# Kernel optimization log

Hardware: AMD Instinct MI355X
Metric: run time of the kernel (lower is better)

The kernel has to match this reference:

```python
import jax, jax.numpy as jnp
import numpy as np
from jax import lax

B, N, C = 4, 20000, 256
NUM_VIEW = 300
NUM_SAMPLE = 1024
EPS_BN = 1e-5


def _grasp_views(n=NUM_VIEW):
    # graspnetAPI generate_grasp_views: spiral points on unit sphere
    phi = (np.sqrt(5.0) - 1.0) / 2.0
    i = np.arange(n)
    z = (2.0 * i + 1.0) / n - 1.0
    r = np.sqrt(np.maximum(1.0 - z * z, 0.0))
    x = r * np.cos(2.0 * np.pi * i * phi)
    y = r * np.sin(2.0 * np.pi * i * phi)
    return jnp.asarray(np.stack([x, y, z], axis=1).astype(np.float32))  # [300,3]

_TEMPLATE_VIEWS = _grasp_views()


def _conv1x1(x, w, b):
    # Conv1d with kernel_size=1: x [B,Cin,N], w [Cout,Cin], b [Cout]
    return jnp.einsum('oc,bcn->bon', w, x) + b[None, :, None]


def _bn_eval(x, g, be, m, v):
    # BatchNorm1d in eval mode (running stats)
    scale = g / jnp.sqrt(v + EPS_BN)
    return x * scale[None, :, None] + (be - m * scale)[None, :, None]


def _masked_fps(xyz, mask, n_samples):
    # Equivalent to compacting valid points, running torch furthest_point_sample,
    # and mapping indices back: run FPS on the full set with invalid points pinned
    # to -inf min-distance so they are never selected. Start = first valid index
    # (index 0 of the compacted set). Tie-breaking matches (order preserved).
    first = jnp.argmax(mask, axis=1)                      # [B]
    init_d = jnp.where(mask, jnp.float32(1e10), -jnp.inf)  # [B,N]

    def step(carry, _):
        dists, last = carry
        p = jnp.take_along_axis(xyz, last[:, None, None], axis=1)  # [B,1,3]
        d = jnp.sum((xyz - p) ** 2, axis=-1)                       # [B,N]
        dists = jnp.minimum(dists, d)
        nxt = jnp.argmax(dists, axis=1)
        return (dists, nxt), nxt

    _, rest = lax.scan(step, (init_d, first), None, length=n_samples - 1)
    return jnp.concatenate([first[None, :], rest], axis=0).T  # [B,S] int


def _viewpoint_to_matrix(towards):
    # batch_viewpoint_params_to_matrix with batch_angle = 0 => R1 = I
    ax = towards  # [M,3]
    ay = jnp.stack([-ax[:, 1], ax[:, 0], jnp.zeros_like(ax[:, 0])], axis=-1)
    deg = jnp.sum(ay * ay, axis=-1, keepdims=True) == 0
    ay = jnp.where(deg, jnp.array([0.0, 1.0, 0.0], dtype=ax.dtype), ay)
    nx = ax / jnp.linalg.norm(ax, axis=-1, keepdims=True)
    ny = ay / jnp.linalg.norm(ay, axis=-1, keepdims=True)
    nz = jnp.cross(nx, ny)
    return jnp.stack([nx, ny, nz], axis=-1)  # [M,3,3], axes as columns


def setup_inputs() -> dict:
    key = jax.random.key(0)
    ks = jax.random.split(key, 18)

    def w(k, shape, s=0.05):
        return jax.random.normal(k, shape, jnp.float32) * s

    return dict(
        seed_xyz=jax.random.normal(ks[0], (B, N, 3), jnp.float32),
        seed_features=jax.random.normal(ks[1], (B, C, N), jnp.float32),
        gh_w1=w(ks[2], (C, C)), gh_b1=w(ks[3], (C,), 0.01),
        gh_g=1.0 + 0.1 * jax.random.normal(ks[4], (C,), jnp.float32),
        gh_be=w(ks[5], (C,), 0.01),
        gh_m=w(ks[6], (C,), 0.1),
        gh_v=jax.random.uniform(ks[7], (C,), jnp.float32, 0.5, 1.5),
        gh_w2=w(ks[8], (3, C)), gh_b2=w(ks[9], (3,), 0.01),
        c1_w=w(ks[10], (C, C)), c1_b=w(ks[11], (C,), 0.01),
        bn_g=1.0 + 0.1 * jax.random.normal(ks[12], (C,), jnp.float32),
        bn_b=w(ks[13], (C,), 0.01),
        bn_m=w(ks[14], (C,), 0.1),
        bn_v=jax.random.uniform(ks[15], (C,), jnp.float32, 0.5, 1.5),
        c2_w=w(ks[16], (3, C)), c2_b=w(ks[17], (3,), 0.01),
    )


def reference(seed_xyz, seed_features, gh_w1, gh_b1, gh_g, gh_be, gh_m, gh_v,
              gh_w2, gh_b2, c1_w, c1_b, bn_g, bn_b, bn_m, bn_v, c2_w, c2_b):
    # graspable head: conv-BN-ReLU-conv -> [B,3,N]
    h = jax.nn.relu(_bn_eval(_conv1x1(seed_features, gh_w1, gh_b1), gh_g, gh_be, gh_m, gh_v))
    graspable = _conv1x1(h, gh_w2, gh_b2)
    objectness_score = graspable[:, :2]          # [B,2,N]
    graspness_score = graspable[:, 2]            # [B,N]

    obj_mask = jnp.argmax(objectness_score, axis=1) == 1
    gmask = (graspness_score > 0.1) & obj_mask   # [B,N] bool

    graspable_inds = _masked_fps(seed_xyz, gmask, NUM_SAMPLE)            # [B,S]
    graspable_xyz = jnp.take_along_axis(seed_xyz, graspable_inds[:, :, None], axis=1)   # [B,S,3]
    graspable_features = jnp.take_along_axis(seed_features, graspable_inds[:, None, :], axis=2)  # [B,C,S]
    fp2_graspness = jnp.take_along_axis(graspness_score, graspable_inds, axis=1)        # [B,S]

    f = jax.nn.relu(_bn_eval(_conv1x1(graspable_features, c1_w, c1_b), bn_g, bn_b, bn_m, bn_v))
    vp_xyz = jnp.transpose(_conv1x1(f, c2_w, c2_b), (0, 2, 1))  # [B,S,3]

    # cosine similarity against 300 template views (torch clamps each norm at 1e-8)
    vn = vp_xyz / jnp.maximum(jnp.linalg.norm(vp_xyz, axis=-1, keepdims=True), 1e-8)
    tn = _TEMPLATE_VIEWS / jnp.maximum(jnp.linalg.norm(_TEMPLATE_VIEWS, axis=-1, keepdims=True), 1e-8)
    cos = jnp.einsum('bsd,vd->bsv', vn, tn)      # [B,S,300]
    top_view_inds = jnp.argmax(cos, axis=2)      # [B,S]

    vp_rot = _viewpoint_to_matrix(-vp_xyz.reshape(-1, 3)).reshape(B, NUM_SAMPLE, 3, 3)

    return (objectness_score, graspness_score, graspable_xyz, graspable_inds,
            graspable_features, fp2_graspness, vp_xyz, top_view_inds, vp_rot)
```

## Files before the change

kernel.cpp:

```cpp
#include <hip/hip_runtime.h>
#include <hip/hip_bf16.h>
#include <math.h>

static constexpr int BB = 4;
static constexpr int NN = 20000;
static constexpr int CC = 256;
static constexpr int SS = 1024;
static constexpr int NV = 300;

static constexpr size_t O0 = 0;
static constexpr size_t O1 = O0 + (size_t)BB*2*NN;
static constexpr size_t O2 = O1 + (size_t)BB*NN;
static constexpr size_t O3 = O2 + (size_t)BB*SS*3;
static constexpr size_t O4 = O3 + (size_t)BB*SS;
static constexpr size_t O5 = O4 + (size_t)BB*CC*SS;
static constexpr size_t O6 = O5 + (size_t)BB*SS;
static constexpr size_t O7 = O6 + (size_t)BB*SS*3;
static constexpr size_t O8 = O7 + (size_t)BB*SS;

typedef float v2f __attribute__((ext_vector_type(2)));

static constexpr int TN = 64;
static constexpr int KC = 32;
static constexpr int SW_LD = 260;
static constexpr int PS_LD = 68;

__global__ __launch_bounds__(256, 2) void gemm_fused(
    const float* __restrict__ X,
    const float* __restrict__ W1, const float* __restrict__ B1v,
    const float* __restrict__ Gv, const float* __restrict__ BEv,
    const float* __restrict__ Mv, const float* __restrict__ Vv,
    const float* __restrict__ W2, const float* __restrict__ B2v,
    float* __restrict__ o0, float* __restrict__ o1)
{
    __shared__ alignas(16) char smem_raw[KC*SW_LD*4 + KC*TN*4];
    float* sW   = (float*)smem_raw;
    float* sF   = (float*)(smem_raw + KC*SW_LD*4);
    float* psum = (float*)smem_raw;
    float* gout = (float*)(smem_raw + 3*32*PS_LD*4);

    const int t  = threadIdx.x;
    const int b  = blockIdx.y;
    const int n0 = blockIdx.x * TN;
    const int tm = t & 31;
    const int tn = t >> 5;

    const float* Xb = X + (size_t)b * CC * NN;

    float acc[8][8];
#pragma unroll
    for (int i = 0; i < 8; ++i)
#pragma unroll
        for (int j = 0; j < 8; ++j) acc[i][j] = 0.f;

    for (int k0 = 0; k0 < CC; k0 += KC) {
#pragma unroll
        for (int r = 0; r < (CC*KC)/256; ++r) {
            int idx = r*256 + t;
            int m  = idx >> 5;
            int kk = idx & 31;
            sW[kk*SW_LD + m] = W1[m*CC + k0 + kk];
        }
#pragma unroll
        for (int r = 0; r < (KC*TN)/256; ++r) {
            int idx = r*256 + t;
            int kk = idx >> 6;
            int j  = idx & 63;
            int col = n0 + j;
            float v = 0.f;
            if (col < NN) v = Xb[(size_t)(k0+kk)*NN + col];
            sF[kk*TN + j] = v;
        }
        __syncthreads();
#pragma unroll 8
        for (int kk = 0; kk < KC; ++kk) {
            const float4 a0 = *(const float4*)(sW + kk*SW_LD + tm*8);
            const float4 a1 = *(const float4*)(sW + kk*SW_LD + tm*8 + 4);
            const float4 f0 = *(const float4*)(sF + kk*TN + tn*8);
            const float4 f1 = *(const float4*)(sF + kk*TN + tn*8 + 4);
            float av[8] = {a0.x,a0.y,a0.z,a0.w,a1.x,a1.y,a1.z,a1.w};
            float bv[8] = {f0.x,f0.y,f0.z,f0.w,f1.x,f1.y,f1.z,f1.w};
#pragma unroll
            for (int i = 0; i < 8; ++i)
#pragma unroll
                for (int j = 0; j < 8; ++j)
                    acc[i][j] = fmaf(av[i], bv[j], acc[i][j]);
        }
        __syncthreads();
    }

    float part[3][8];
#pragma unroll
    for (int r = 0; r < 3; ++r)
#pragma unroll
        for (int j = 0; j < 8; ++j) part[r][j] = 0.f;

#pragma unroll
    for (int i = 0; i < 8; ++i) {
        int m = tm*8 + i;
        float scale = __fdiv_rn(Gv[m], __fsqrt_rn(__fadd_rn(Vv[m], 1e-5f)));
        float shift = __fsub_rn(BEv[m], __fmul_rn(Mv[m], scale));
        float w0 = W2[m], w1 = W2[CC + m], w2 = W2[2*CC + m];
        float b1m = B1v[m];
#pragma unroll
        for (int j = 0; j < 8; ++j) {
            float x = __fadd_rn(acc[i][j], b1m);
            float y = __fadd_rn(__fmul_rn(x, scale), shift);
            float h = y > 0.f ? y : 0.f;
            part[0][j] = fmaf(w0, h, part[0][j]);
            part[1][j] = fmaf(w1, h, part[1][j]);
            part[2][j] = fmaf(w2, h, part[2][j]);
        }
    }
#pragma unroll
    for (int r = 0; r < 3; ++r) {
        float4 p0 = {part[r][0], part[r][1], part[r][2], part[r][3]};
        float4 p1 = {part[r][4], part[r][5], part[r][6], part[r][7]};
        *(float4*)(psum + (r*32 + tm)*PS_LD + tn*8)     = p0;
        *(float4*)(psum + (r*32 + tm)*PS_LD + tn*8 + 4) = p1;
    }
    __syncthreads();
    if (t < 192) {
        int r = t >> 6, col = t & 63;
        float s = 0.f;
#pragma unroll
        for (int w = 0; w < 32; ++w) s = __fadd_rn(s, psum[(r*32 + w)*PS_LD + col]);
        float tot = __fadd_rn(s, B2v[r]);
        gout[r*64 + col] = tot;
    }
    __syncthreads();
    if (t < 64) {
        int n = n0 + t;
        if (n < NN) {
            o0[(size_t)b*2*NN + n]      = gout[t];
            o0[(size_t)b*2*NN + NN + n] = gout[64 + t];
            o1[(size_t)b*NN + n]        = gout[128 + t];
        }
    }
}

static constexpr int FPS_T = 256;
static constexpr int KAMAX = 20;
static constexpr int CAPA  = FPS_T * KAMAX;

template<int CTRL>
__device__ __forceinline__ unsigned long long dpp_umax(unsigned long long k) {
    int lo = __builtin_amdgcn_update_dpp(0, (int)(unsigned)k,         CTRL, 0xf, 0xf, false);
    int hi = __builtin_amdgcn_update_dpp(0, (int)(unsigned)(k >> 32), CTRL, 0xf, 0xf, false);
    unsigned long long ok = ((unsigned long long)(unsigned)hi << 32) | (unsigned)lo;
    return ok > k ? ok : k;
}

__device__ __forceinline__ unsigned long long wave_umax_dpp(unsigned long long k) {
    k = dpp_umax<0x111>(k);
    k = dpp_umax<0x112>(k);
    k = dpp_umax<0x114>(k);
    k = dpp_umax<0x118>(k);
    k = dpp_umax<0x142>(k);
    k = dpp_umax<0x143>(k);
    return k;
}

__device__ __forceinline__ unsigned long long pack_key(float v, int i) {
    unsigned long long k = (((unsigned long long)__float_as_uint(v)) << 32)
                         | (unsigned long long)(0xFFFFFFFFu - (unsigned)i);
    return (v == -INFINITY) ? 0ull : k;
}

template<int KP>
__device__ __forceinline__ void fps_scan_loop(
    int cnt, const float* __restrict__ sxyz,
    unsigned long long (*swk)[4], int* __restrict__ whist)
{
#pragma clang fp contract(off)
    const int t = threadIdx.x;
    const int wave = t >> 6, lane = t & 63;

    v2f X2[KP], Y2[KP], Z2[KP], D2[KP];
#pragma unroll
    for (int jp = 0; jp < KP; ++jp) {
        int g0 = t + ((2*jp) << 8);
        int g1 = g0 + 256;
        bool v0 = g0 < cnt, v1 = g1 < cnt;
        float4 wa = v0 ? *(const float4*)&sxyz[g0*4] : make_float4(0.f,0.f,0.f,0.f);
        float4 wb = v1 ? *(const float4*)&sxyz[g1*4] : make_float4(0.f,0.f,0.f,0.f);
        X2[jp][0] = wa.x; X2[jp][1] = wb.x;
        Y2[jp][0] = wa.y; Y2[jp][1] = wb.y;
        Z2[jp][0] = wa.z; Z2[jp][1] = wb.z;
        D2[jp][0] = v0 ? 1e10f : -INFINITY;
        D2[jp][1] = v1 ? 1e10f : -INFINITY;
    }

    float px = sxyz[0], py = sxyz[1], pz = sxyz[2];

    for (int it = 1; it < SS; ++it) {
        float bv = -INFINITY; int bi = 0x7fffffff;
#pragma unroll
        for (int jp = 0; jp < KP; ++jp) {
            v2f dx = X2[jp] - px;
            v2f dy = Y2[jp] - py;
            v2f dz = Z2[jp] - pz;
            v2f xx = dx*dx, yy = dy*dy;
            v2f sxy = xx + yy;
            v2f zz = dz*dz;
            v2f dd = sxy + zz;
            float dn0 = fminf(D2[jp][0], dd[0]);
            float dn1 = fminf(D2[jp][1], dd[1]);
            D2[jp][0] = dn0;
            D2[jp][1] = dn1;
            if (dn0 > bv) { bv = dn0; bi = t + ((2*jp)   << 8); }
            if (dn1 > bv) { bv = dn1; bi = t + ((2*jp+1) << 8); }
        }
        unsigned long long key = wave_umax_dpp(pack_key(bv, bi));
        int par = it & 1;
        if (lane == 63) swk[par][wave] = key;
        __syncthreads();
        const ulonglong2* kp = (const ulonglong2*)&swk[par][0];
        ulonglong2 kA = kp[0], kB = kp[1];
        unsigned long long m0 = kA.x > kA.y ? kA.x : kA.y;
        unsigned long long m1 = kB.x > kB.y ? kB.x : kB.y;
        unsigned long long best = m0 > m1 ? m0 : m1;
        int wi = (int)(0xFFFFFFFFu - (unsigned)(best & 0xFFFFFFFFull));
        float4 w4 = *(const float4*)&sxyz[wi*4];
        px = w4.x; py = w4.y; pz = w4.z;
        if (t == 0) whist[it] = wi;
    }
}

__global__ __launch_bounds__(256, 1) void mega_kernel(
    const float* __restrict__ xyz, const float* __restrict__ feats,
    const float* __restrict__ o0, const float* __restrict__ o1,
    const float* __restrict__ c1w, const float* __restrict__ c1b,
    const float* __restrict__ bng, const float* __restrict__ bnb,
    const float* __restrict__ bnm, const float* __restrict__ bnv,
    const float* __restrict__ c2w, const float* __restrict__ c2b,
    int* __restrict__ corig, float* __restrict__ cxg,
    float* __restrict__ cyg, float* __restrict__ czg,
    float* __restrict__ o2, float* __restrict__ o3, float* __restrict__ o4,
    float* __restrict__ o5, float* __restrict__ o6, float* __restrict__ o7,
    float* __restrict__ o8, int* __restrict__ indsp, int* __restrict__ donep)
{
    __shared__ alignas(16) char sm[86272];
    const int t = threadIdx.x;
    const int wave = t >> 6, lane = t & 63;

    if (blockIdx.x < BB) {
        const int b = blockIdx.x;
        const size_t bofs = (size_t)b*NN;
        float* sxyz = (float*)sm;
        int*   whist = (int*)(sm + 81920);
        unsigned long long (*swk)[4] = (unsigned long long (*)[4])(sm + 86016);
        int*   wsum  = (int*)(sm + 86080);
        int*   smisc = (int*)(sm + 86096);

        if (t == 0) smisc[0] = 0;
        __syncthreads();
        const float* ob0 = o0 + (size_t)b*2*NN;
        const float* ob1 = o1 + (size_t)b*NN;
        for (int base = 0; base < NN; base += 256) {
            int i = base + t;
            bool valid = i < NN;
            float g1 = valid ? ob1[i]      : 0.f;
            float v0 = valid ? ob0[i]      : 0.f;
            float v1 = valid ? ob0[NN + i] : 0.f;
            bool m = valid && (g1 > 0.1f) && (v1 > v0);
            unsigned long long bal = __ballot(m);
            int pre = __popcll(bal & ((1ull << lane) - 1ull));
            if (lane == 0) wsum[wave] = __popcll(bal);
            __syncthreads();
            int offs = smisc[0];
            int tilesum = wsum[0] + wsum[1] + wsum[2] + wsum[3];
            for (int ww = 0; ww < wave; ++ww) offs += wsum[ww];
            if (m) {
                int pos = offs + pre;
                float x = xyz[(bofs + i)*3 + 0];
                float y = xyz[(bofs + i)*3 + 1];
                float z = xyz[(bofs + i)*3 + 2];
                corig[bofs + pos] = i;
                cxg[bofs + pos] = x; cyg[bofs + pos] = y; czg[bofs + pos] = z;
                if (pos < CAPA) {
                    float4 w4 = {x, y, z, 0.f};
                    *(float4*)&sxyz[pos*4] = w4;
                }
            }
            __syncthreads();
            if (t == 0) smisc[0] += tilesum;
        }
        __syncthreads();
        const int cnt = smisc[0];

        float* o3b = o3 + (size_t)b*SS;
        int*   oib = indsp + (size_t)b*SS;

        if (cnt <= 0) {
            for (int s = t; s < SS; s += FPS_T) { o3b[s] = 0.f; oib[s] = 0; }
            __syncthreads();
            if (t == 0) {
                __threadfence();
                __hip_atomic_fetch_add(donep, 1, __ATOMIC_RELEASE, __HIP_MEMORY_SCOPE_AGENT);
            }
            return;
        }

        if (t == 0) whist[0] = 0;
        __syncthreads();

        if (cnt <= CAPA) {
            int kat2 = ((cnt + 255) >> 8);
            kat2 = (kat2 + 1) & ~1;
            int kpn = kat2 >> 1;
            switch (kpn) {
                case 1:  fps_scan_loop<1 >(cnt, sxyz, swk, whist); break;
                case 2:  fps_scan_loop<2 >(cnt, sxyz, swk, whist); break;
                case 3:  fps_scan_loop<3 >(cnt, sxyz, swk, whist); break;
                case 4:  fps_scan_loop<4 >(cnt, sxyz, swk, whist); break;
                case 5:  fps_scan_loop<5 >(cnt, sxyz, swk, whist); break;
                case 6:  fps_scan_loop<6 >(cnt, sxyz, swk, whist); break;
                case 7:  fps_scan_loop<7 >(cnt, sxyz, swk, whist); break;
                case 8:  fps_scan_loop<8 >(cnt, sxyz, swk, whist); break;
                case 9:  fps_scan_loop<9 >(cnt, sxyz, swk, whist); break;
                default: fps_scan_loop<10>(cnt, sxyz, swk, whist); break;
            }
        } else {
            float* Dl = sxyz;
            for (int g = t; g < cnt; g += FPS_T) Dl[g] = 1e10f;
            __syncthreads();
            float px = cxg[bofs], py = cyg[bofs], pz = czg[bofs];
            for (int it = 1; it < SS; ++it) {
                float bv = -INFINITY; int bi = 0x7fffffff;
                for (int g = t; g < cnt; g += FPS_T) {
                    float dx = __fsub_rn(cxg[bofs + g], px);
                    float dy = __fsub_rn(cyg[bofs + g], py);
                    float dz = __fsub_rn(czg[bofs + g], pz);
                    float d  = __fadd_rn(__fadd_rn(__fmul_rn(dx,dx), __fmul_rn(dy,dy)), __fmul_rn(dz,dz));
                    float dn = fminf(Dl[g], d);
                    Dl[g] = dn;
                    if (dn > bv) { bv = dn; bi = g; }
                }
                unsigned long long key = wave_umax_dpp(pack_key(bv, bi));
                int par = it & 1;
                if (lane == 63) swk[par][wave] = key;
                __syncthreads();
                const ulonglong2* kp = (const ulonglong2*)&swk[par][0];
                ulonglong2 kA = kp[0], kB = kp[1];
                unsigned long long m0 = kA.x > kA.y ? kA.x : kA.y;
                unsigned long long m1 = kB.x > kB.y ? kB.x : kB.y;
                unsigned long long best = m0 > m1 ? m0 : m1;
                int wi = (int)(0xFFFFFFFFu - (unsigned)(best & 0xFFFFFFFFull));
                px = cxg[bofs + wi]; py = cyg[bofs + wi]; pz = czg[bofs + wi];
                if (t == 0) whist[it] = wi;
            }
        }

        __syncthreads();
        for (int s = t; s < SS; s += FPS_T) {
            int wi  = whist[s];
            int org = corig[bofs + wi];
            oib[s] = org;
            o3b[s] = (float)org;
        }
        __syncthreads();
        if (t == 0) {
            __threadfence();
            __hip_atomic_fetch_add(donep, 1, __ATOMIC_RELEASE, __HIP_MEMORY_SCOPE_AGENT);
        }
        return;
    }

    {
        int* smisc = (int*)(sm + 86096);
        if (t == 0) smisc[1] = 0;
        __syncthreads();
        float a = 1.0f + (float)t * 1e-6f, bmul = 1.0000001f, c = 0.f;
        for (int iter = 0; iter < (1 << 22); ++iter) {
#pragma unroll
            for (int u = 0; u < 16; ++u) c = fmaf(a, bmul, c);
            __builtin_amdgcn_s_sleep(8);
            if (t == 0 && (iter & 7) == 0) {
                if (__hip_atomic_load(donep, __ATOMIC_RELAXED, __HIP_MEMORY_SCOPE_AGENT) >= BB)
                    *(volatile int*)&smisc[1] = 1;
            }
            if (*(volatile int*)&smisc[1]) break;
        }
        ((volatile float*)sm)[32 + (t & 31)] = c;
        __syncthreads();
        (void)__hip_atomic_load(donep, __ATOMIC_ACQUIRE, __HIP_MEMORY_SCOPE_AGENT);
    }

    const int wid = blockIdx.x - BB;

    if (wid < 64) {
        const int bi = wid >> 4;
        const int n0 = (wid & 15) << 6;
        float* sW   = (float*)sm;
        float* sF   = (float*)(sm + KC*SW_LD*4);
        float* psum = (float*)sm;
        float* gout = (float*)(sm + 3*32*PS_LD*4);
        float* tv   = (float*)(sm + KC*SW_LD*4);
        int*   sIdx = (int*)(sm + 81920);

        if (t < 64) sIdx[t] = indsp[(bi << 10) + n0 + t];
        __syncthreads();

        const int tm = t & 31;
        const int tn = t >> 5;

        float acc[8][8];
#pragma unroll
        for (int i = 0; i < 8; ++i)
#pragma unroll
            for (int j = 0; j < 8; ++j) acc[i][j] = 0.f;

        for (int k0 = 0; k0 < CC; k0 += KC) {
#pragma unroll
            for (int r = 0; r < (CC*KC)/256; ++r) {
                int idx = r*256 + t;
                int m  = idx >> 5;
                int kk = idx & 31;
                sW[kk*SW_LD + m] = c1w[m*CC + k0 + kk];
            }
#pragma unroll
            for (int r = 0; r < (KC*TN)/256; ++r) {
                int idx = r*256 + t;
                int kk = idx >> 6;
                int j  = idx & 63;
                sF[kk*TN + j] = feats[((size_t)bi*CC + k0 + kk)*NN + sIdx[j]];
            }
            __syncthreads();
#pragma unroll 8
            for (int kk = 0; kk < KC; ++kk) {
                const float4 a0 = *(const float4*)(sW + kk*SW_LD + tm*8);
                const float4 a1 = *(const float4*)(sW + kk*SW_LD + tm*8 + 4);
                const float4 f0 = *(const float4*)(sF + kk*TN + tn*8);
                const float4 f1 = *(const float4*)(sF + kk*TN + tn*8 + 4);
                float av[8] = {a0.x,a0.y,a0.z,a0.w,a1.x,a1.y,a1.z,a1.w};
                float bv[8] = {f0.x,f0.y,f0.z,f0.w,f1.x,f1.y,f1.z,f1.w};
#pragma unroll
                for (int i = 0; i < 8; ++i)
#pragma unroll
                    for (int j = 0; j < 8; ++j)
                        acc[i][j] = fmaf(av[i], bv[j], acc[i][j]);
            }
            __syncthreads();
        }

        float part[3][8];
#pragma unroll
        for (int r = 0; r < 3; ++r)
#pragma unroll
            for (int j = 0; j < 8; ++j) part[r][j] = 0.f;

#pragma unroll
        for (int i = 0; i < 8; ++i) {
            int m = tm*8 + i;
            float scale = __fdiv_rn(bng[m], __fsqrt_rn(__fadd_rn(bnv[m], 1e-5f)));
            float shift = __fsub_rn(bnb[m], __fmul_rn(bnm[m], scale));
            float w0 = c2w[m], w1 = c2w[CC + m], w2 = c2w[2*CC + m];
            float b1m = c1b[m];
#pragma unroll
            for (int j = 0; j < 8; ++j) {
                float x = __fadd_rn(acc[i][j], b1m);
                float y = __fadd_rn(__fmul_rn(x, scale), shift);
                float h = y > 0.f ? y : 0.f;
                part[0][j] = fmaf(w0, h, part[0][j]);
                part[1][j] = fmaf(w1, h, part[1][j]);
                part[2][j] = fmaf(w2, h, part[2][j]);
            }
        }
#pragma unroll
        for (int r = 0; r < 3; ++r) {
            float4 p0 = {part[r][0], part[r][1], part[r][2], part[r][3]};
            float4 p1 = {part[r][4], part[r][5], part[r][6], part[r][7]};
            *(float4*)(psum + (r*32 + tm)*PS_LD + tn*8)     = p0;
            *(float4*)(psum + (r*32 + tm)*PS_LD + tn*8 + 4) = p1;
        }
        __syncthreads();
        if (t < 192) {
            int r = t >> 6, col = t & 63;
            float s = 0.f;
#pragma unroll
            for (int w = 0; w < 32; ++w) s = __fadd_rn(s, psum[(r*32 + w)*PS_LD + col]);
            float tot = __fadd_rn(s, c2b[r]);
            gout[r*64 + col] = tot;
            o6[((size_t)bi*SS + n0 + col)*3 + r] = tot;
        }
        __syncthreads();
        for (int i = t; i < NV; i += 256) {
            double phi = (sqrt(5.0) - 1.0) * 0.5;
            double zd  = (2.0*(double)i + 1.0)/300.0 - 1.0;
            double rr  = sqrt(fmax(1.0 - zd*zd, 0.0));
            double ang = 2.0 * 3.14159265358979323846 * (double)i * phi;
            float fx = (float)(rr * cos(ang));
            float fy = (float)(rr * sin(ang));
            float fz = (float)zd;
            float nr = __fsqrt_rn(__fadd_rn(__fadd_rn(__fmul_rn(fx,fx), __fmul_rn(fy,fy)), __fmul_rn(fz,fz)));
            float dn = fmaxf(nr, 1e-8f);
            tv[i]       = __fdiv_rn(fx, dn);
            tv[NV + i]  = __fdiv_rn(fy, dn);
            tv[2*NV + i]= __fdiv_rn(fz, dn);
        }
        __syncthreads();
        if (t < 64) {
            int col = t;
            int sg = bi*SS + n0 + col;
            float vx = gout[col], vy = gout[64 + col], vz = gout[128 + col];

            float nr = __fsqrt_rn(__fadd_rn(__fadd_rn(__fmul_rn(vx,vx), __fmul_rn(vy,vy)), __fmul_rn(vz,vz)));
            float dn = fmaxf(nr, 1e-8f);
            float ux = __fdiv_rn(vx, dn), uy = __fdiv_rn(vy, dn), uz = __fdiv_rn(vz, dn);
            float best = -INFINITY; int bidx = 0;
            for (int v = 0; v < NV; ++v) {
                float cde = __fadd_rn(__fadd_rn(__fmul_rn(ux, tv[v]), __fmul_rn(uy, tv[NV+v])), __fmul_rn(uz, tv[2*NV+v]));
                if (cde > best) { best = cde; bidx = v; }
            }
            o7[sg] = (float)bidx;

            float axx = -vx, axy = -vy, axz = -vz;
            float ayx = vy, ayy = -vx, ayz = 0.f;
            float s2 = __fadd_rn(__fadd_rn(__fmul_rn(ayx,ayx), __fmul_rn(ayy,ayy)), 0.f);
            if (s2 == 0.f) { ayx = 0.f; ayy = 1.f; ayz = 0.f; }
            float an = __fsqrt_rn(__fadd_rn(__fadd_rn(__fmul_rn(axx,axx), __fmul_rn(axy,axy)), __fmul_rn(axz,axz)));
            float nx0 = __fdiv_rn(axx, an), nx1 = __fdiv_rn(axy, an), nx2 = __fdiv_rn(axz, an);
            float bn2 = __fsqrt_rn(__fadd_rn(__fadd_rn(__fmul_rn(ayx,ayx), __fmul_rn(ayy,ayy)), __fmul_rn(ayz,ayz)));
            float ny0 = __fdiv_rn(ayx, bn2), ny1 = __fdiv_rn(ayy, bn2), ny2 = __fdiv_rn(ayz, bn2);
            float nz0 = __fsub_rn(__fmul_rn(nx1, ny2), __fmul_rn(nx2, ny1));
            float nz1 = __fsub_rn(__fmul_rn(nx2, ny0), __fmul_rn(nx0, ny2));
            float nz2 = __fsub_rn(__fmul_rn(nx0, ny1), __fmul_rn(nx1, ny0));
            size_t o = (size_t)sg * 9;
            o8[o+0] = nx0; o8[o+1] = ny0; o8[o+2] = nz0;
            o8[o+3] = nx1; o8[o+4] = ny1; o8[o+5] = nz1;
            o8[o+6] = nx2; o8[o+7] = ny2; o8[o+8] = nz2;
        }
    } else {
        const int NQ = (BB*CC*SS) / 4;
        for (int q = (wid - 64)*256 + t; q < NQ; q += 188*256) {
            int e = q << 2;
            int b = e >> 18;
            int r = e & ((1 << 18) - 1);
            int c = r >> 10;
            int s = r & 1023;
            int4 i4 = *(const int4*)&indsp[(b << 10) + s];
            const float* fb = feats + ((size_t)b*CC + c)*NN;
            float4 v = { fb[i4.x], fb[i4.y], fb[i4.z], fb[i4.w] };
            *(float4*)&o4[e] = v;
            if (c == 0) {
                const float* gb = o1 + (size_t)b*NN;
                float4 g4 = { gb[i4.x], gb[i4.y], gb[i4.z], gb[i4.w] };
                *(float4*)&o5[(b << 10) + s] = g4;
                const float* xb = xyz + (size_t)b*NN*3;
                float o2buf[12];
                int ii[4] = { i4.x, i4.y, i4.z, i4.w };
#pragma unroll
                for (int k = 0; k < 4; ++k) {
                    o2buf[k*3+0] = xb[(size_t)ii[k]*3 + 0];
                    o2buf[k*3+1] = xb[(size_t)ii[k]*3 + 1];
                    o2buf[k*3+2] = xb[(size_t)ii[k]*3 + 2];
                }
                float* dst = o2 + ((size_t)(b << 10) + s)*3;
                *(float4*)&dst[0] = *(float4*)&o2buf[0];
                *(float4*)&dst[4] = *(float4*)&o2buf[4];
                *(float4*)&dst[8] = *(float4*)&o2buf[8];
            }
        }
    }
}

extern "C" void kernel_launch(void* const* d_in, const int* in_sizes, int n_in,
                              void* d_out, int out_size, void* d_ws, size_t ws_size,
                              hipStream_t stream) {
    const float* xyz   = (const float*)d_in[0];
    const float* feats = (const float*)d_in[1];
    const float* gh_w1 = (const float*)d_in[2];
    const float* gh_b1 = (const float*)d_in[3];
    const float* gh_g  = (const float*)d_in[4];
    const float* gh_be = (const float*)d_in[5];
    const float* gh_m  = (const float*)d_in[6];
    const float* gh_v  = (const float*)d_in[7];
    const float* gh_w2 = (const float*)d_in[8];
    const float* gh_b2 = (const float*)d_in[9];
    const float* c1_w  = (const float*)d_in[10];
    const float* c1_b  = (const float*)d_in[11];
    const float* bn_g  = (const float*)d_in[12];
    const float* bn_b  = (const float*)d_in[13];
    const float* bn_m  = (const float*)d_in[14];
    const float* bn_v  = (const float*)d_in[15];
    const float* c2_w  = (const float*)d_in[16];
    const float* c2_b  = (const float*)d_in[17];

    float* out = (float*)d_out;
    float* o0 = out + O0;
    float* o1 = out + O1;
    float* o2 = out + O2;
    float* o3 = out + O3;
    float* o4 = out + O4;
    float* o5 = out + O5;
    float* o6 = out + O6;
    float* o7 = out + O7;
    float* o8 = out + O8;

    char* ws = (char*)d_ws;
    size_t off = 0;
    auto take = [&](size_t bytes) -> char* {
        char* p = ws + off;
        off = (off + bytes + 255) & ~(size_t)255;
        return p;
    };
    int*   corig = (int*)take((size_t)BB*NN*4);
    float* cx    = (float*)take((size_t)BB*NN*4);
    float* cy    = (float*)take((size_t)BB*NN*4);
    float* cz    = (float*)take((size_t)BB*NN*4);
    int*   indsp = (int*)take((size_t)BB*SS*4);
    int*   donep = (int*)take(64);

    gemm_fused<<<dim3((NN + TN - 1)/TN, BB), 256, 0, stream>>>(
        feats, gh_w1, gh_b1, gh_g, gh_be, gh_m, gh_v, gh_w2, gh_b2, o0, o1);

    hipMemsetAsync(donep, 0, 4, stream);
    mega_kernel<<<dim3(256), 256, 0, stream>>>(
        xyz, feats, o0, o1,
        c1_w, c1_b, bn_g, bn_b, bn_m, bn_v, c2_w, c2_b,
        corig, cx, cy, cz,
        o2, o3, o4, o5, o6, o7, o8, indsp, donep);
}
```

Before: 1.113 ms.

## Double-buffer gemm_fused shared tiles with register prefetch and packed FMA

Restructures the first fused GEMM's main loop to use two shared-memory buffers with a K-chunk of 16. Global loads for the next chunk go into registers while the current chunk is being computed, which overlaps memory latency with math and removes one barrier per iteration. Loads are widened to float4, and the accumulators become float2 vectors so the compiler can emit packed FMA instructions. The costs are more registers for the prefetch and more shared memory per block, which could lower occupancy under launch_bounds(256,2).

Result: faster. 944.2 us (-15.2%).

```diff
diff --git a/kernel.cpp b/kernel.cpp
--- a/kernel.cpp
+++ b/kernel.cpp
@@ -25,6 +25,11 @@
 static constexpr int SW_LD = 260;
 static constexpr int PS_LD = 68;
 
+static constexpr int G1_TN  = 64;
+static constexpr int G1_KC  = 16;
+static constexpr int G1_LD  = 260;
+static constexpr int G1_BUF = G1_KC*G1_LD + G1_KC*G1_TN;
+
 __global__ __launch_bounds__(256, 2) void gemm_fused(
     const float* __restrict__ X,
     const float* __restrict__ W1, const float* __restrict__ B1v,
@@ -33,59 +38,99 @@
     const float* __restrict__ W2, const float* __restrict__ B2v,
     float* __restrict__ o0, float* __restrict__ o1)
 {
-    __shared__ alignas(16) char smem_raw[KC*SW_LD*4 + KC*TN*4];
-    float* sW   = (float*)smem_raw;
-    float* sF   = (float*)(smem_raw + KC*SW_LD*4);
-    float* psum = (float*)smem_raw;
-    float* gout = (float*)(smem_raw + 3*32*PS_LD*4);
+    __shared__ alignas(16) float smem[2*G1_BUF];
+    float* psum = smem;
+    float* gout = smem + 3*32*PS_LD;
 
     const int t  = threadIdx.x;
     const int b  = blockIdx.y;
-    const int n0 = blockIdx.x * TN;
+    const int n0 = blockIdx.x * G1_TN;
     const int tm = t & 31;
     const int tn = t >> 5;
-
     const float* Xb = X + (size_t)b * CC * NN;
-
-    float acc[8][8];
+    const bool full = (n0 + G1_TN <= NN);
+
+    v2f acc2[8][4];
 #pragma unroll
     for (int i = 0; i < 8; ++i)
 #pragma unroll
-        for (int j = 0; j < 8; ++j) acc[i][j] = 0.f;
-
-    for (int k0 = 0; k0 < CC; k0 += KC) {
-#pragma unroll
-        for (int r = 0; r < (CC*KC)/256; ++r) {
-            int idx = r*256 + t;
-            int m  = idx >> 5;
-            int kk = idx & 31;
-            sW[kk*SW_LD + m] = W1[m*CC + k0 + kk];
-        }
-#pragma unroll
-        for (int r = 0; r < (KC*TN)/256; ++r) {
-            int idx = r*256 + t;
-            int kk = idx >> 6;
-            int j  = idx & 63;
-            int col = n0 + j;
-            float v = 0.f;
-            if (col < NN) v = Xb[(size_t)(k0+kk)*NN + col];
-            sF[kk*TN + j] = v;
-        }
-        __syncthreads();
+        for (int jp = 0; jp < 4; ++jp) acc2[i][jp] = (v2f){0.f, 0.f};
+
+    float4 wreg[4];
+    float4 xreg;
+
+    auto stage_load = [&](int k0) {
+#pragma unroll
+        for (int r = 0; r < 4; ++r) {
+            int f  = r*1024 + t*4;
+            int m  = f >> 4;
+            int kk = f & 15;
+            wreg[r] = *(const float4*)&W1[(size_t)m*CC + k0 + kk];
+        }
+        int fx = t*4;
+        int kk = fx >> 6;
+        int j  = fx & 63;
+        if (full) {
+            xreg = *(const float4*)&Xb[(size_t)(k0+kk)*NN + n0 + j];
+        } else {
+            float tmp[4];
+#pragma unroll
+            for (int u = 0; u < 4; ++u) {
+                int col = n0 + j + u;
+                tmp[u] = (col < NN) ? Xb[(size_t)(k0+kk)*NN + col] : 0.f;
+            }
+            xreg = make_float4(tmp[0], tmp[1], tmp[2], tmp[3]);
+        }
+    };
+
+    auto stage_write = [&](float* sWb, float* sFb) {
+#pragma unroll
+        for (int r = 0; r < 4; ++r) {
+            int f  = r*1024 + t*4;
+            int m  = f >> 4;
+            int kk = f & 15;
+            float tmp[4] = {wreg[r].x, wreg[r].y, wreg[r].z, wreg[r].w};
+#pragma unroll
+            for (int u = 0; u < 4; ++u)
+                sWb[(kk+u)*G1_LD + m] = tmp[u];
+        }
+        int fx = t*4;
+        int kk = fx >> 6;
+        int j  = fx & 63;
+        *(float4*)&sFb[kk*G1_TN + j] = xreg;
+    };
+
+    stage_load(0);
+    stage_write(smem, smem + G1_KC*G1_LD);
+    __syncthreads();
+
+    for (int c = 0; c < CC/G1_KC; ++c) {
+        const int cur = c & 1;
+        float* base_cur = smem + cur*G1_BUF;
+        float* base_nxt = smem + (cur^1)*G1_BUF;
+
+        if (c + 1 < CC/G1_KC) stage_load((c+1)*G1_KC);
+
+        const float* sWc = base_cur;
+        const float* sFc = base_cur + G1_KC*G1_LD;
 #pragma unroll 8
-        for (int kk = 0; kk < KC; ++kk) {
-            const float4 a0 = *(const float4*)(sW + kk*SW_LD + tm*8);
-            const float4 a1 = *(const float4*)(sW + kk*SW_LD + tm*8 + 4);
-            const float4 f0 = *(const float4*)(sF + kk*TN + tn*8);
-            const float4 f1 = *(const float4*)(sF + kk*TN + tn*8 + 4);
+        for (int kk = 0; kk < G1_KC; ++kk) {
+            const float4 a0 = *(const float4*)(sWc + kk*G1_LD + tm*8);
+            const float4 a1 = *(const float4*)(sWc + kk*G1_LD + tm*8 + 4);
+            const float4 f0 = *(const float4*)(sFc + kk*G1_TN + tn*8);
+            const float4 f1 = *(const float4*)(sFc + kk*G1_TN + tn*8 + 4);
             float av[8] = {a0.x,a0.y,a0.z,a0.w,a1.x,a1.y,a1.z,a1.w};
-            float bv[8] = {f0.x,f0.y,f0.z,f0.w,f1.x,f1.y,f1.z,f1.w};
-#pragma unroll
-            for (int i = 0; i < 8; ++i)
-#pragma unroll
-                for (int j = 0; j < 8; ++j)
-                    acc[i][j] = fmaf(av[i], bv[j], acc[i][j]);
-        }
+            v2f bv2[4] = {{f0.x,f0.y},{f0.z,f0.w},{f1.x,f1.y},{f1.z,f1.w}};
+#pragma unroll
+            for (int i = 0; i < 8; ++i) {
+                v2f ai = {av[i], av[i]};
+#pragma unroll
+                for (int jp = 0; jp < 4; ++jp)
+                    acc2[i][jp] += ai * bv2[jp];
+            }
+        }
+
+        if (c + 1 < CC/G1_KC) stage_write(base_nxt, base_nxt + G1_KC*G1_LD);
         __syncthreads();
     }
 
@@ -104,7 +149,7 @@
         float b1m = B1v[m];
 #pragma unroll
         for (int j = 0; j < 8; ++j) {
-            float x = __fadd_rn(acc[i][j], b1m);
+            float x = __fadd_rn(acc2[i][j>>1][j&1], b1m);
             float y = __fadd_rn(__fmul_rn(x, scale), shift);
             float h = y > 0.f ? y : 0.f;
             part[0][j] = fmaf(w0, h, part[0][j]);
@@ -612,7 +657,7 @@
     int*   indsp = (int*)take((size_t)BB*SS*4);
     int*   donep = (int*)take(64);
 
-    gemm_fused<<<dim3((NN + TN - 1)/TN, BB), 256, 0, stream>>>(
+    gemm_fused<<<dim3((NN + G1_TN - 1)/G1_TN, BB), 256, 0, stream>>>(
         feats, gh_w1, gh_b1, gh_g, gh_be, gh_m, gh_v, gh_w2, gh_b2, o0, o1);
 
     hipMemsetAsync(donep, 0, 4, stream);
```
